# Performance work log

Measured on AMD Instinct MI355X. Metric: run time of the kernel, lower is better.

Reference implementation:

```python
import jax, jax.numpy as jnp
import numpy as np


def _rotate_half(x):
    x1, x2 = jnp.split(x, 2, axis=-1)
    return jnp.concatenate((-x2, x1), axis=-1)


def setup_inputs() -> dict:
    key = jax.random.key(0)
    ks = jax.random.split(key, 8)
    B, T, C, H = 2, 2048, 1024, 16
    Dh = C // H
    x = jax.random.normal(ks[0], (B, T, C), dtype=jnp.float32)
    # RoPE tables (T, head_dim)
    inv_freq = 1.0 / (10000.0 ** (np.arange(0, Dh, 2, dtype=np.float32) / Dh))
    pos = np.arange(T, dtype=np.float32)
    freqs = np.einsum('t,f->tf', pos, inv_freq)
    emb = np.concatenate([freqs, freqs], axis=-1)
    cos = jnp.asarray(np.cos(emb), dtype=jnp.float32)
    sin = jnp.asarray(np.sin(emb), dtype=jnp.float32)
    # causal mask: 1 where attending allowed, 0 elsewhere
    mask = jnp.tril(jnp.ones((T, T), dtype=jnp.int32))
    s = 0.02
    Wq = jax.random.normal(ks[1], (C, C), dtype=jnp.float32) * s
    Wk = jax.random.normal(ks[2], (C, C), dtype=jnp.float32) * s
    Wv = jax.random.normal(ks[3], (C, C), dtype=jnp.float32) * s
    Wo = jax.random.normal(ks[4], (C, C), dtype=jnp.float32) * s
    return {"x": x, "cos": cos, "sin": sin, "mask": mask, "n_heads": H,
            "Wq": Wq, "Wk": Wk, "Wv": Wv, "Wo": Wo}


def reference(x, cos, sin, mask, n_heads, Wq, Wk, Wv, Wo):
    B, T, C = x.shape
    H = n_heads
    Dh = C // H
    scale = Dh ** (-0.5)
    # projections (torch Linear: x @ W.T), reshape to (B, H, T, Dh)
    def proj(W):
        return (x @ W.T).reshape(B, T, H, Dh).transpose(0, 2, 1, 3)
    q, k, v = proj(Wq), proj(Wk), proj(Wv)
    # RoPE: cos/sin broadcast as (1, 1, T, Dh)
    c = cos[None, None]
    s = sin[None, None]
    q = q * c + _rotate_half(q) * s
    k = k * c + _rotate_half(k) * s
    att = jnp.einsum('bhtd,bhsd->bhts', q, k) * scale
    att = jnp.where(mask == 0, -jnp.inf, att)
    att = jax.nn.softmax(att, axis=-1)
    out = jnp.einsum('bhts,bhsd->bhtd', att, v)
    out = out.transpose(0, 2, 1, 3).reshape(B, T, C)
    return out @ Wo.T
```

## Files before the change

kernel.cpp:

```cpp
#include <hip/hip_runtime.h>
#include <stdint.h>

#define B_   2
#define T_   2048
#define C_   1024
#define H_   16
#define BT   4096
#define KDIM 1024

typedef unsigned short u16;
typedef __attribute__((ext_vector_type(8))) __bf16 bf16v8;
typedef __attribute__((ext_vector_type(4))) float f32x4;
typedef __attribute__((ext_vector_type(16))) float f32x16;
typedef __attribute__((ext_vector_type(4))) unsigned int u32x4;

#define MFMA16(a, b, c) __builtin_amdgcn_mfma_f32_16x16x32_bf16((a), (b), (c), 0, 0, 0)
#define MFMA32(a, b, c) __builtin_amdgcn_mfma_f32_32x32x16_bf16((a), (b), (c), 0, 0, 0)

#define BARRIER() do { asm volatile("" ::: "memory"); \
                       __builtin_amdgcn_s_barrier();  \
                       asm volatile("" ::: "memory"); } while (0)

__device__ __forceinline__ u16 f2bf(float f) {
  __bf16 h = (__bf16)f;
  union { __bf16 h; u16 u; } v; v.h = h;
  return v.u;
}

__device__ __forceinline__ void gload16(const void* g, void* l) {
  __builtin_amdgcn_global_load_lds((__attribute__((address_space(1))) void*)g,
                                   (__attribute__((address_space(3))) void*)l,
                                   16, 0, 0);
}

__global__ __launch_bounds__(256) void cvt_f32_bf16(const float* __restrict__ in,
                                                    u16* __restrict__ out, int n) {
  int i = (blockIdx.x * 256 + threadIdx.x) * 4;
  if (i + 3 < n) {
    float4 v = *(const float4*)(in + i);
    ushort4 o;
    o.x = f2bf(v.x); o.y = f2bf(v.y); o.z = f2bf(v.z); o.w = f2bf(v.w);
    *(ushort4*)(out + i) = o;
  }
}

__global__ __launch_bounds__(256) void cvt_weights(
    const float* __restrict__ wq, const float* __restrict__ wk,
    const float* __restrict__ wv, const float* __restrict__ wo,
    u16* __restrict__ qkv_dst, u16* __restrict__ o_dst) {
  const int bid = blockIdx.x;
  const int sel = bid >> 10;
  const float* src = (sel == 0) ? wq : (sel == 1) ? wk : (sel == 2) ? wv : wo;
  u16* dst = (sel < 3) ? (qkv_dst + sel * 1048576) : o_dst;
  const int i = ((bid & 1023) * 256 + threadIdx.x) * 4;
  float4 v = *(const float4*)(src + i);
  ushort4 o;
  o.x = f2bf(v.x); o.y = f2bf(v.y); o.z = f2bf(v.z); o.w = f2bf(v.w);
  *(ushort4*)(dst + i) = o;
}

template<int EPI, int NN>
__global__ __launch_bounds__(256, 2) void gemm128(
    const u16* __restrict__ A, const u16* __restrict__ Bm,
    float* __restrict__ Cf,
    u16* __restrict__ qo, u16* __restrict__ ko, u16* __restrict__ vt,
    const float* __restrict__ cosT, const float* __restrict__ sinT)
{
  __shared__ __align__(16) u16 As[2][128 * 64];
  __shared__ __align__(16) u16 Bs[2][128 * 64];
  const int tid = threadIdx.x;
  const int lane = tid & 63;
  const int w = tid >> 6;
  const int wm = w >> 1, wn = w & 1;
  const int lmod = lane & 15, ldiv = lane >> 4;

  constexpr int NBX = NN / 128;
  constexpr int XG_BY = (NBX == 24) ? 8 : 4;
  constexpr int XG_BX = (NBX == 24) ? 12 : 8;
  const int x = blockIdx.x & 7;
  const int i = blockIdx.x >> 3;
  const int gy = (NBX == 24) ? (x >> 1) : x;
  const int gx = (NBX == 24) ? (x & 1) : 0;
  const int by = gy * XG_BY + (i % XG_BY);
  const int bx = gx * XG_BX + (i / XG_BY);
  const int row0 = by * 128, col0 = bx * 128;

  const int srow = tid >> 3;
  const int sswz = ((tid & 7) * 16) ^ ((srow & 7) << 4);
  const char* Abase = (const char*)A + (size_t)(row0 + srow) * (KDIM * 2) + sswz;
  const char* Bbase = (const char*)Bm + (size_t)(col0 + srow) * (KDIM * 2) + sswz;
  const int ldst = (tid & 192) * 16;

  auto stage = [&](int buf, int t) {
    const int kb = t * 128;
#pragma unroll
    for (int c = 0; c < 4; ++c)
      gload16(Abase + (size_t)c * 32 * (KDIM * 2) + kb,
              (char*)As[buf] + c * 4096 + ldst);
#pragma unroll
    for (int c = 0; c < 4; ++c)
      gload16(Bbase + (size_t)c * 32 * (KDIM * 2) + kb,
              (char*)Bs[buf] + c * 4096 + ldst);
  };

  f32x4 acc[4][4] = {};
  stage(0, 0);

  for (int t = 0; t < KDIM / 64; ++t) {
    const int cur = t & 1;
    BARRIER();
    if (t + 1 < KDIM / 64) {
      stage(cur ^ 1, t + 1);
      asm volatile("s_waitcnt vmcnt(8)" ::: "memory");
    } else {
      asm volatile("s_waitcnt vmcnt(0)" ::: "memory");
    }
    BARRIER();

    bf16v8 af[4][2], bfr[4][2];
#pragma unroll
    for (int mf = 0; mf < 4; ++mf) {
      const int rr = wm * 64 + mf * 16 + lmod;
#pragma unroll
      for (int kc = 0; kc < 2; ++kc)
        af[mf][kc] = *(const bf16v8*)((const char*)As[cur] + rr * 128 +
                          ((kc * 64 + ldiv * 16) ^ ((rr & 7) << 4)));
    }
#pragma unroll
    for (int nf = 0; nf < 4; ++nf) {
      const int rr = wn * 64 + nf * 16 + lmod;
#pragma unroll
      for (int kc = 0; kc < 2; ++kc)
        bfr[nf][kc] = *(const bf16v8*)((const char*)Bs[cur] + rr * 128 +
                          ((kc * 64 + ldiv * 16) ^ ((rr & 7) << 4)));
    }
#pragma unroll
    for (int kc = 0; kc < 2; ++kc)
#pragma unroll
      for (int mf = 0; mf < 4; ++mf)
#pragma unroll
        for (int nf = 0; nf < 4; ++nf)
          acc[mf][nf] = MFMA16(af[mf][kc], bfr[nf][kc], acc[mf][nf]);
  }

  if (EPI == 0) {
#pragma unroll
    for (int mf = 0; mf < 4; ++mf) {
      const int mbase = row0 + wm * 64 + mf * 16 + ldiv * 4;
#pragma unroll
      for (int nf = 0; nf < 4; ++nf) {
        const int n = col0 + wn * 64 + nf * 16 + lmod;
#pragma unroll
        for (int r = 0; r < 4; ++r)
          Cf[(size_t)(mbase + r) * NN + n] = acc[mf][nf][r];
      }
    }
  } else {
    const int nb = col0 + wn * 64;
    const int proj = nb >> 10;
    const int hh = (nb & 1023) >> 6;
    if (proj < 2) {
      u16* dst = proj ? ko : qo;
#pragma unroll
      for (int mf = 0; mf < 4; ++mf) {
#pragma unroll
        for (int r = 0; r < 4; ++r) {
          const int m = row0 + wm * 64 + mf * 16 + ldiv * 4 + r;
          const int b = m >> 11, t = m & 2047;
          u16* drow = dst + ((size_t)(b * H_ + hh) * T_ + t) * 64;
#pragma unroll
          for (int nf = 0; nf < 4; ++nf) {
            const int d = nf * 16 + lmod;
            const float cs = cosT[t * 64 + d];
            const float sn = sinT[t * 64 + d];
            const float other = (nf < 2) ? acc[mf][nf + 2][r] : acc[mf][nf - 2][r];
            float val = (nf < 2) ? (acc[mf][nf][r] * cs - other * sn)
                                 : (acc[mf][nf][r] * cs + other * sn);
            if (proj == 0) val *= 0.18033688011112042f;
            drow[d] = f2bf(val);
          }
        }
      }
    } else {
      BARRIER();
      char* scr = (char*)As + w * 8192;
#pragma unroll
      for (int nf = 0; nf < 4; ++nf)
#pragma unroll
        for (int mf = 0; mf < 4; ++mf)
#pragma unroll
          for (int rp = 0; rp < 2; ++rp) {
            const int dd = nf * 16 + lmod;
            const int t0 = mf * 16 + ldiv * 4 + rp * 2;
            const uint32_t pk = (uint32_t)f2bf(acc[mf][nf][rp * 2]) |
                                ((uint32_t)f2bf(acc[mf][nf][rp * 2 + 1]) << 16);
            *(uint32_t*)(scr + ((dd * 128 + t0 * 2) ^ ((dd & 7) << 4))) = pk;
          }
      __syncthreads();
      const int trow = row0 + wm * 64;
      const int bb = trow >> 11, tl = trow & 2047;
#pragma unroll
      for (int j = 0; j < 8; ++j) {
        const int dd = j * 8 + (lane >> 3);
        const int c = lane & 7;
        const u32x4 vv = *(const u32x4*)(scr + ((dd * 128 + c * 16) ^ ((dd & 7) << 4)));
        u16* drow = vt + ((size_t)((bb * H_ + hh) * 64 + dd)) * T_ + tl;
        *(u32x4*)((char*)drow + c * 16) = vv;
      }
    }
  }
}

__global__ __launch_bounds__(256, 2) void attn_fwd3(
    const u16* __restrict__ Q, const u16* __restrict__ K,
    const u16* __restrict__ Vt, u16* __restrict__ O)
{
  __shared__ __align__(16) u16 Kl[2][64 * 64];
  __shared__ __align__(16) u16 Vl[2][64 * 64];
  const int xcd = blockIdx.x & 7;
  const int idx = blockIdx.x >> 3;
  const int h   = idx & 1;
  const int j   = idx >> 1;
  const int bh  = xcd * 4 + (j & 3);
  const int cr  = j >> 2;
  const int chunk = h ? (15 - cr) : cr;
  const int qb0 = chunk * 128;
  const int nblk = 2 * chunk + 2;

  const int tid = threadIdx.x, lane = tid & 63, w = tid >> 6;
  const int l31 = lane & 31, hi = lane >> 5;
  const int qrow = qb0 + w * 32;

  bf16v8 qf[4];
  {
    const u16* qp = Q + ((size_t)bh * T_ + qrow + l31) * 64 + hi * 8;
    qf[0] = *(const bf16v8*)(qp);
    qf[1] = *(const bf16v8*)(qp + 16);
    qf[2] = *(const bf16v8*)(qp + 32);
    qf[3] = *(const bf16v8*)(qp + 48);
  }

  float m2 = -1e30f, lsum = 0.f;
  f32x16 oacc0 = {}, oacc1 = {};

  const int scolb = (tid & 7) * 16;
  const int ldst = (tid & 192) * 16;

  auto stage = [&](int buf, int t) {
    const int s0 = t << 6;
#pragma unroll
    for (int c = 0; c < 2; ++c) {
      const int row = (c * 256 + tid) >> 3;
      const int sw = scolb ^ ((row & 7) << 4);
      gload16((const char*)(K + ((size_t)bh * T_ + s0 + row) * 64) + sw,
              (char*)Kl[buf] + c * 4096 + ldst);
    }
#pragma unroll
    for (int c = 0; c < 2; ++c) {
      const int row = (c * 256 + tid) >> 3;
      const int sw = scolb ^ ((row & 7) << 4);
      gload16((const char*)(Vt + ((size_t)(bh * 64 + row)) * T_ + s0) + sw,
              (char*)Vl[buf] + c * 4096 + ldst);
    }
  };

  auto substep = [&](int cur, int sub, int s0_sub) {
    bf16v8 kf[4], vf[4];
#pragma unroll
    for (int c = 0; c < 4; ++c) {
      const int row = sub * 32 + l31;
      kf[c] = *(const bf16v8*)((const char*)Kl[cur] + row * 128 +
                  ((c * 32 + hi * 16) ^ ((row & 7) << 4)));
    }
#pragma unroll
    for (int db = 0; db < 2; ++db)
#pragma unroll
      for (int kg = 0; kg < 2; ++kg) {
        const int row = db * 32 + l31;
        vf[db * 2 + kg] = *(const bf16v8*)((const char*)Vl[cur] + row * 128 +
                  ((sub * 64 + kg * 32 + hi * 16) ^ ((row & 7) << 4)));
      }
    f32x16 s = {};
    s = MFMA32(kf[0], qf[0], s);
    s = MFMA32(kf[1], qf[1], s);
    s = MFMA32(kf[2], qf[2], s);
    s = MFMA32(kf[3], qf[3], s);
    if (s0_sub + 31 > qrow) {
#pragma unroll
      for (int r = 0; r < 16; ++r) {
        const int key = s0_sub + (r & 3) + 8 * (r >> 2) + 4 * hi;
        if (key > qrow + l31) s[r] = -1e30f;
      }
    }
    float pmax = s[0];
#pragma unroll
    for (int r = 1; r < 16; ++r) pmax = fmaxf(pmax, s[r]);
    pmax = fmaxf(pmax, __shfl_xor(pmax, 32));
    if (!__all(pmax <= m2 + 11.5416f)) {
      const float mnew = fmaxf(m2, pmax);
      const float rs = __builtin_amdgcn_exp2f(m2 - mnew);
      lsum *= rs;
#pragma unroll
      for (int r = 0; r < 16; ++r) { oacc0[r] *= rs; oacc1[r] *= rs; }
      m2 = mnew;
    }
    float p[16]; float ts = 0.f;
#pragma unroll
    for (int r = 0; r < 16; ++r) {
      p[r] = __builtin_amdgcn_exp2f(s[r] - m2);
      ts += p[r];
    }
    ts += __shfl_xor(ts, 32);
    lsum += ts;
    uint32_t o[8];
#pragma unroll
    for (int jj = 0; jj < 8; ++jj) {
      const int r0 = 4 * (jj >> 1) + 2 * (jj & 1);
      uint32_t d;
      asm("v_cvt_pk_bf16_f32 %0, %1, %2" : "=v"(d) : "v"(p[r0]), "v"(p[r0 + 1]));
      o[jj] = d;
    }
    uint32_t po[8];
#pragma unroll
    for (int jj = 0; jj < 8; ++jj) po[jj] = __shfl_xor(o[jj], 32);
#pragma unroll
    for (int kg = 0; kg < 2; ++kg) {
      u32x4 fr;
      fr.x = hi ? po[4 * kg + 2] : o[4 * kg + 0];
      fr.y = hi ? po[4 * kg + 3] : o[4 * kg + 1];
      fr.z = hi ? o[4 * kg + 2] : po[4 * kg + 0];
      fr.w = hi ? o[4 * kg + 3] : po[4 * kg + 1];
      const bf16v8 pf = __builtin_bit_cast(bf16v8, fr);
      oacc0 = MFMA32(vf[kg], pf, oacc0);
      oacc1 = MFMA32(vf[2 + kg], pf, oacc1);
    }
  };

  stage(0, 0);
  for (int t = 0; t < nblk; ++t) {
    const int cur = t & 1;
    BARRIER();
    if (t + 1 < nblk) {
      stage(cur ^ 1, t + 1);
      asm volatile("s_waitcnt vmcnt(4)" ::: "memory");
    } else {
      asm volatile("s_waitcnt vmcnt(0)" ::: "memory");
    }
    BARRIER();
#pragma unroll
    for (int sub = 0; sub < 2; ++sub) {
      const int s0_sub = t * 64 + sub * 32;
      if (s0_sub <= qrow + 31) substep(cur, sub, s0_sub);
    }
  }

  BARRIER();
  char* scr = (char*)Kl + w * 4096;
  const float inv = 1.f / lsum;
#pragma unroll
  for (int r2 = 0; r2 < 8; ++r2) {
    const int r = r2 * 2;
    const int dd = (r & 3) + 8 * (r >> 2) + 4 * hi;
    const uint32_t pk0 = (uint32_t)f2bf(oacc0[r] * inv) |
                         ((uint32_t)f2bf(oacc0[r + 1] * inv) << 16);
    *(uint32_t*)(scr + ((l31 * 128 + dd * 2) ^ ((l31 & 7) << 4))) = pk0;
    const uint32_t pk1 = (uint32_t)f2bf(oacc1[r] * inv) |
                         ((uint32_t)f2bf(oacc1[r + 1] * inv) << 16);
    *(uint32_t*)(scr + ((l31 * 128 + (dd + 32) * 2) ^ ((l31 & 7) << 4))) = pk1;
  }
  __syncthreads();
  const int b = bh >> 4, hh = bh & 15;
  const int qq = lane >> 1, cc = lane & 1;
  u16* orow = O + ((size_t)(b * T_ + qrow + qq)) * C_ + hh * 64 + cc * 32;
#pragma unroll
  for (int jj = 0; jj < 4; ++jj) {
    const u32x4 vv = *(const u32x4*)(scr + ((qq * 128 + cc * 64 + jj * 16) ^ ((qq & 7) << 4)));
    *(u32x4*)((char*)orow + jj * 16) = vv;
  }
}

extern "C" void kernel_launch(void* const* d_in, const int* in_sizes, int n_in,
                              void* d_out, int out_size, void* d_ws, size_t ws_size,
                              hipStream_t stream) {
  const float* x    = (const float*)d_in[0];
  const float* cosT = (const float*)d_in[1];
  const float* sinT = (const float*)d_in[2];
  const float* Wq = (const float*)d_in[5];
  const float* Wk = (const float*)d_in[6];
  const float* Wv = (const float*)d_in[7];
  const float* Wo = (const float*)d_in[8];
  float* out = (float*)d_out;

  char* ws = (char*)d_ws;
  u16* xb   = (u16*)(ws);
  u16* wqkv = (u16*)(ws + 8388608);
  u16* wo   = (u16*)(ws + 14680064);
  u16* q    = (u16*)(ws + 16777216);
  u16* k    = (u16*)(ws + 25165824);
  u16* vt   = (u16*)(ws + 33554432);
  u16* aout = (u16*)(ws + 41943040);

  cvt_f32_bf16<<<4096, 256, 0, stream>>>(x, xb, BT * C_);
  cvt_weights<<<4096, 256, 0, stream>>>(Wq, Wk, Wv, Wo, wqkv, wo);

  gemm128<1, 3072><<<768, 256, 0, stream>>>(xb, wqkv, nullptr,
                                            q, k, vt, cosT, sinT);
  attn_fwd3<<<512, 256, 0, stream>>>(q, k, vt, aout);
  gemm128<0, 1024><<<256, 256, 0, stream>>>(aout, wo, out,
                                            nullptr, nullptr, nullptr,
                                            nullptr, nullptr);
}
```

Measured before the change: 123.7 us.

## Split attention into 64-row query blocks and use permlane32 swaps for softmax

The attention kernel now runs 1024 blocks of 128 threads (two waves) covering 64 query rows each, in place of 512 blocks of 256 threads covering 128 rows. K/V staging is adjusted so each thread issues four loads per tensor, and the wait count is raised to match. Cross-half-wave reductions and the P-fragment exchange use permlane32_swap where available in place of ds_bpermute-based shuffles, and the row max and sum are computed as tree reductions. Smaller blocks should give finer causal load balancing and more blocks per CU, at the cost of reloading each K/V tile for twice as many query blocks.

Result: slower. 128.2 us (+3.6%).

```diff
diff --git a/kernel.cpp b/kernel.cpp
--- a/kernel.cpp
+++ b/kernel.cpp
@@ -13,6 +13,7 @@
 typedef __attribute__((ext_vector_type(4))) float f32x4;
 typedef __attribute__((ext_vector_type(16))) float f32x16;
 typedef __attribute__((ext_vector_type(4))) unsigned int u32x4;
+typedef __attribute__((ext_vector_type(2))) unsigned int u32x2;
 
 #define MFMA16(a, b, c) __builtin_amdgcn_mfma_f32_16x16x32_bf16((a), (b), (c), 0, 0, 0)
 #define MFMA32(a, b, c) __builtin_amdgcn_mfma_f32_32x32x16_bf16((a), (b), (c), 0, 0, 0)
@@ -25,6 +26,18 @@
   __bf16 h = (__bf16)f;
   union { __bf16 h; u16 u; } v; v.h = h;
   return v.u;
+}
+
+__device__ __forceinline__ void xhalf(uint32_t a, uint32_t b,
+                                      uint32_t& lo, uint32_t& hi) {
+#if defined(__has_builtin) && __has_builtin(__builtin_amdgcn_permlane32_swap)
+  u32x2 r = __builtin_amdgcn_permlane32_swap(a, b, false, false);
+  lo = r.x; hi = r.y;
+#else
+  const bool upper = (threadIdx.x & 32) != 0;
+  lo = upper ? __shfl_xor(b, 32) : a;
+  hi = upper ? b : __shfl_xor(a, 32);
+#endif
 }
 
 __device__ __forceinline__ void gload16(const void* g, void* l) {
@@ -211,21 +224,21 @@
   }
 }
 
-__global__ __launch_bounds__(256, 2) void attn_fwd3(
+__global__ __launch_bounds__(128, 2) void attn_fwd3(
     const u16* __restrict__ Q, const u16* __restrict__ K,
     const u16* __restrict__ Vt, u16* __restrict__ O)
 {
   __shared__ __align__(16) u16 Kl[2][64 * 64];
   __shared__ __align__(16) u16 Vl[2][64 * 64];
   const int xcd = blockIdx.x & 7;
-  const int idx = blockIdx.x >> 3;
-  const int h   = idx & 1;
-  const int j   = idx >> 1;
-  const int bh  = xcd * 4 + (j & 3);
-  const int cr  = j >> 2;
-  const int chunk = h ? (15 - cr) : cr;
-  const int qb0 = chunk * 128;
-  const int nblk = 2 * chunk + 2;
+  const int i   = blockIdx.x >> 3;
+  const int bh  = xcd * 4 + (i & 3);
+  const int rest = i >> 2;
+  const int hgt = rest & 1;
+  const int cr  = rest >> 1;
+  const int chunk = hgt ? (31 - cr) : cr;
+  const int qb0 = chunk * 64;
+  const int nblk = chunk + 1;
 
   const int tid = threadIdx.x, lane = tid & 63, w = tid >> 6;
   const int l31 = lane & 31, hi = lane >> 5;
@@ -244,23 +257,23 @@
   f32x16 oacc0 = {}, oacc1 = {};
 
   const int scolb = (tid & 7) * 16;
-  const int ldst = (tid & 192) * 16;
+  const int ldst = (tid & 64) * 16;
 
   auto stage = [&](int buf, int t) {
     const int s0 = t << 6;
 #pragma unroll
-    for (int c = 0; c < 2; ++c) {
-      const int row = (c * 256 + tid) >> 3;
+    for (int c = 0; c < 4; ++c) {
+      const int row = c * 16 + (tid >> 3);
       const int sw = scolb ^ ((row & 7) << 4);
       gload16((const char*)(K + ((size_t)bh * T_ + s0 + row) * 64) + sw,
-              (char*)Kl[buf] + c * 4096 + ldst);
-    }
-#pragma unroll
-    for (int c = 0; c < 2; ++c) {
-      const int row = (c * 256 + tid) >> 3;
+              (char*)Kl[buf] + c * 2048 + ldst);
+    }
+#pragma unroll
+    for (int c = 0; c < 4; ++c) {
+      const int row = c * 16 + (tid >> 3);
       const int sw = scolb ^ ((row & 7) << 4);
       gload16((const char*)(Vt + ((size_t)(bh * 64 + row)) * T_ + s0) + sw,
-              (char*)Vl[buf] + c * 4096 + ldst);
+              (char*)Vl[buf] + c * 2048 + ldst);
     }
   };
 
@@ -292,10 +305,17 @@
         if (key > qrow + l31) s[r] = -1e30f;
       }
     }
-    float pmax = s[0];
-#pragma unroll
-    for (int r = 1; r < 16; ++r) pmax = fmaxf(pmax, s[r]);
-    pmax = fmaxf(pmax, __shfl_xor(pmax, 32));
+    float t8[8];
+#pragma unroll
+    for (int r = 0; r < 8; ++r) t8[r] = fmaxf(s[r], s[r + 8]);
+    float t4a = fmaxf(t8[0], t8[4]), t4b = fmaxf(t8[1], t8[5]);
+    float t4c = fmaxf(t8[2], t8[6]), t4d = fmaxf(t8[3], t8[7]);
+    float pmax = fmaxf(fmaxf(t4a, t4b), fmaxf(t4c, t4d));
+    {
+      uint32_t lo, hh2;
+      xhalf(__builtin_bit_cast(uint32_t, pmax), __builtin_bit_cast(uint32_t, pmax), lo, hh2);
+      pmax = fmaxf(__builtin_bit_cast(float, lo), __builtin_bit_cast(float, hh2));
+    }
     if (!__all(pmax <= m2 + 11.5416f)) {
       const float mnew = fmaxf(m2, pmax);
       const float rs = __builtin_amdgcn_exp2f(m2 - mnew);
@@ -304,13 +324,20 @@
       for (int r = 0; r < 16; ++r) { oacc0[r] *= rs; oacc1[r] *= rs; }
       m2 = mnew;
     }
-    float p[16]; float ts = 0.f;
-#pragma unroll
-    for (int r = 0; r < 16; ++r) {
-      p[r] = __builtin_amdgcn_exp2f(s[r] - m2);
-      ts += p[r];
-    }
-    ts += __shfl_xor(ts, 32);
+    float p[16];
+#pragma unroll
+    for (int r = 0; r < 16; ++r) p[r] = __builtin_amdgcn_exp2f(s[r] - m2);
+    float a8[8];
+#pragma unroll
+    for (int r = 0; r < 8; ++r) a8[r] = p[r] + p[r + 8];
+    float a4a = a8[0] + a8[4], a4b = a8[1] + a8[5];
+    float a4c = a8[2] + a8[6], a4d = a8[3] + a8[7];
+    float ts = (a4a + a4b) + (a4c + a4d);
+    {
+      uint32_t lo, hh2;
+      xhalf(__builtin_bit_cast(uint32_t, ts), __builtin_bit_cast(uint32_t, ts), lo, hh2);
+      ts = __builtin_bit_cast(float, lo) + __builtin_bit_cast(float, hh2);
+    }
     lsum += ts;
     uint32_t o[8];
 #pragma unroll
@@ -320,16 +347,13 @@
       asm("v_cvt_pk_bf16_f32 %0, %1, %2" : "=v"(d) : "v"(p[r0]), "v"(p[r0 + 1]));
       o[jj] = d;
     }
-    uint32_t po[8];
-#pragma unroll
-    for (int jj = 0; jj < 8; ++jj) po[jj] = __shfl_xor(o[jj], 32);
 #pragma unroll
     for (int kg = 0; kg < 2; ++kg) {
+      uint32_t f0, f1, f2, f3;
+      xhalf(o[4 * kg + 0], o[4 * kg + 2], f0, f2);
+      xhalf(o[4 * kg + 1], o[4 * kg + 3], f1, f3);
       u32x4 fr;
-      fr.x = hi ? po[4 * kg + 2] : o[4 * kg + 0];
-      fr.y = hi ? po[4 * kg + 3] : o[4 * kg + 1];
-      fr.z = hi ? o[4 * kg + 2] : po[4 * kg + 0];
-      fr.w = hi ? o[4 * kg + 3] : po[4 * kg + 1];
+      fr.x = f0; fr.y = f1; fr.z = f2; fr.w = f3;
       const bf16v8 pf = __builtin_bit_cast(bf16v8, fr);
       oacc0 = MFMA32(vf[kg], pf, oacc0);
       oacc1 = MFMA32(vf[2 + kg], pf, oacc1);
@@ -342,7 +366,7 @@
     BARRIER();
     if (t + 1 < nblk) {
       stage(cur ^ 1, t + 1);
-      asm volatile("s_waitcnt vmcnt(4)" ::: "memory");
+      asm volatile("s_waitcnt vmcnt(8)" ::: "memory");
     } else {
       asm volatile("s_waitcnt vmcnt(0)" ::: "memory");
     }
@@ -405,7 +429,7 @@
 
   gemm128<1, 3072><<<768, 256, 0, stream>>>(xb, wqkv, nullptr,
                                             q, k, vt, cosT, sinT);
-  attn_fwd3<<<512, 256, 0, stream>>>(q, k, vt, aout);
+  attn_fwd3<<<1024, 128, 0, stream>>>(q, k, vt, aout);
   gemm128<0, 1024><<<256, 256, 0, stream>>>(aout, wo, out,
                                             nullptr, nullptr, nullptr,
                                             nullptr, nullptr);
```
